# Optimization experiments

Hardware: AMD Instinct MI355X
Metric: run time of the kernel (lower is better)

## Reference

```python
import jax, jax.numpy as jnp
import numpy as np

IOU_THRESHOLD = 0.5
NEG_POS_RATIO = 3
CONF_WEIGHT = 1.0
BBOX_WEIGHT = 1.0
COUNT_WEIGHT = 0.2
B, A, G = 16, 65536, 32


def _make_boxes(key, shape, max_size):
    kc, ks = jax.random.split(key)
    centers = jax.random.uniform(kc, shape[:-1] + (2,))
    sizes = jax.random.uniform(ks, shape[:-1] + (2,)) * max_size + 0.02
    return jnp.concatenate([centers - sizes / 2, centers + sizes / 2], axis=-1)


def setup_inputs() -> dict:
    key = jax.random.key(0)
    k1, k2, k3, k4 = jax.random.split(key, 4)
    bbox_pred = _make_boxes(k1, (B, A, 4), 0.15)
    conf_pred = jax.random.uniform(k2, (B, A)) * 0.98 + 0.01  # valid probs for BCE
    anchors = _make_boxes(k3, (A, 4), 0.15)
    gt_boxes = _make_boxes(k4, (B, G, 4), 0.3)
    return {"bbox_pred": bbox_pred, "conf_pred": conf_pred, "anchors": anchors, "gt_boxes": gt_boxes}


def _bce(p, t):
    # torch BCELoss: clamps log terms at -100
    logp = jnp.maximum(jnp.log(p), -100.0)
    log1mp = jnp.maximum(jnp.log1p(-p), -100.0)
    return -(t * logp + (1.0 - t) * log1mp)


def _smooth_l1(x, y):
    d = jnp.abs(x - y)
    return jnp.where(d < 1.0, 0.5 * d * d, d - 0.5)


def _center_size(b):
    return jnp.concatenate([(b[:, :2] + b[:, 2:]) / 2, b[:, 2:] - b[:, :2]], axis=1)


def _iou(anchors, gt):  # [A,4],[G,4] -> [A,G]
    lt = jnp.maximum(anchors[:, None, :2], gt[None, :, :2])
    rb = jnp.minimum(anchors[:, None, 2:], gt[None, :, 2:])
    wh = jnp.clip(rb - lt, 0.0)
    inter = wh[..., 0] * wh[..., 1]
    area_a = (anchors[:, 2] - anchors[:, 0]) * (anchors[:, 3] - anchors[:, 1])
    area_g = (gt[:, 2] - gt[:, 0]) * (gt[:, 3] - gt[:, 1])
    union = area_a[:, None] + area_g[None, :] - inter
    return inter / (union + 1e-6)


def _per_image(bbox_p, conf_p, gt, anchors):
    ious = _iou(anchors, gt)                      # [A,G]
    best_gt_iou = ious.max(axis=1)                # [A]
    best_gt_idx = ious.argmax(axis=1)             # [A]
    best_anchor_idx = ious.argmax(axis=0)         # [G]
    pos = (best_gt_iou > IOU_THRESHOLD).at[best_anchor_idx].set(True)
    num_pos = pos.sum()

    matched = gt[best_gt_idx]                     # [A,4]
    loc = _smooth_l1(_center_size(bbox_p), _center_size(matched)).sum(axis=1)
    loc_loss = jnp.where(pos, loc, 0.0).sum()

    conf_t = pos.astype(conf_p.dtype)
    bce = _bce(conf_p, conf_t)                    # [A]
    neg_bce = jnp.where(pos, 0.0, bce)
    num_neg = jnp.minimum(num_pos * NEG_POS_RATIO, A - num_pos)
    sorted_neg = jnp.sort(neg_bce)[::-1]
    neg_sum = jnp.where(jnp.arange(A) < num_neg, sorted_neg, 0.0).sum()
    pos_sum = jnp.where(pos, bce, 0.0).sum()
    conf_loss = neg_sum + pos_sum

    pred_count = (conf_p > 0.5).sum()
    return loc_loss, conf_loss, num_pos, pred_count, best_gt_iou


def reference(bbox_pred, conf_pred, anchors, gt_boxes):
    loc_l, conf_l, num_pos, pred_cnt, best_gt_iou = jax.vmap(
        _per_image, in_axes=(0, 0, 0, None))(bbox_pred, conf_pred, gt_boxes, anchors)

    # count penalty per image (gt count is fixed at G)
    diff = jnp.abs(pred_cnt - G).astype(jnp.float32)
    penalty = jnp.where(diff <= 3.0, diff * 0.2, 0.6 + 0.2 * jnp.log(jnp.maximum(diff - 2.0, 1.0)))
    total_count_loss = penalty.sum() / B

    npos = jnp.maximum(1, num_pos.sum()).astype(bbox_pred.dtype)
    total_loc_loss = loc_l.sum() / npos
    total_conf_loss = conf_l.sum() / npos

    # torch code uses best_gt_iou from the LAST image only (loop-carried variable)
    bgi = best_gt_iou[-1]
    m = bgi > 0
    cnt = m.sum()
    mean_iou = jnp.where(cnt > 0, jnp.where(m, bgi, 0.0).sum() / jnp.maximum(cnt, 1).astype(bgi.dtype), 0.1)
    iou_quality = jnp.clip(1.0 - mean_iou, 0.1, 0.9)
    dyn_bbox_w = BBOX_WEIGHT * (1.0 + iou_quality)

    total_loss = dyn_bbox_w * total_loc_loss + CONF_WEIGHT * total_conf_loss + COUNT_WEIGHT * total_count_loss
    return total_loss, total_conf_loss, total_loc_loss, total_count_loss, mean_iou
```

## Files before the change

kernel.cpp:

```cpp
#include <hip/hip_runtime.h>
#include <math.h>

#define BB 16
#define AA 65536
#define GG 32

#define OFF_PACKED   0
#define OFF_HIST     4096
#define OFF_NUMPOS   69632
#define OFF_LOCSUM   69696
#define OFF_POSBCE   69760
#define OFF_PREDCNT  69824
#define OFF_NEGSUM   69888
#define OFF_NGT      69952
#define OFF_MIOU_S   70016
#define OFF_MIOU_C   70020
#define OFF_VK       70080
#define MEMSET_BYTES 71680
#define OFF_NEGBCE   2097152

__device__ __forceinline__ float iou_exact(float ax, float ay, float az, float aw,
                                           float area_a,
                                           float gx, float gy, float gz, float gw,
                                           float area_g) {
    float lx = fmaxf(ax, gx), ly = fmaxf(ay, gy);
    float rx = fminf(az, gz), ry = fminf(aw, gw);
    float w = fmaxf(__fsub_rn(rx, lx), 0.0f);
    float h = fmaxf(__fsub_rn(ry, ly), 0.0f);
    float inter = __fmul_rn(w, h);
    float uni = __fsub_rn(__fadd_rn(area_a, area_g), inter);
    return __fdiv_rn(inter, __fadd_rn(uni, 1e-6f));
}

__device__ __forceinline__ float sl1(float x, float y) {
    float d = fabsf(__fsub_rn(x, y));
    return (d < 1.0f) ? __fmul_rn(__fmul_rn(0.5f, d), d) : __fsub_rn(d, 0.5f);
}

__device__ __forceinline__ float loc_term(float4 bp, float4 gb) {
    float pcx = __fmul_rn(__fadd_rn(bp.x, bp.z), 0.5f);
    float pcy = __fmul_rn(__fadd_rn(bp.y, bp.w), 0.5f);
    float pw = __fsub_rn(bp.z, bp.x), ph = __fsub_rn(bp.w, bp.y);
    float gcx = __fmul_rn(__fadd_rn(gb.x, gb.z), 0.5f);
    float gcy = __fmul_rn(__fadd_rn(gb.y, gb.w), 0.5f);
    float gw = __fsub_rn(gb.z, gb.x), gh = __fsub_rn(gb.w, gb.y);
    return __fadd_rn(__fadd_rn(__fadd_rn(sl1(pcx, gcx), sl1(pcy, gcy)), sl1(pw, gw)), sl1(ph, gh));
}

__global__ __launch_bounds__(256) void k_main(const float4* __restrict__ bbox,
                                              const float* __restrict__ conf,
                                              const float4* __restrict__ anchors,
                                              const float4* __restrict__ gt,
                                              unsigned long long* __restrict__ packed,
                                              float* __restrict__ neg_bce,
                                              int* __restrict__ hist0,
                                              int* __restrict__ num_pos,
                                              float* __restrict__ loc_sum,
                                              float* __restrict__ posbce,
                                              int* __restrict__ pred_cnt,
                                              float* __restrict__ miou_s,
                                              int* __restrict__ miou_c) {
    const int b = blockIdx.y, t = threadIdx.x;
    const int base = blockIdx.x * 1024;
    __shared__ unsigned long long red[4][GG];
    __shared__ int sh[256];
    __shared__ float sloc[4], spb[4], sms[4];
    __shared__ int snp[4], spc[4], smc[4];
    sh[t] = 0;
    float4 an[4]; float aa[4]; float bi[4]; int bix[4]; int aidx[4];
#pragma unroll
    for (int j = 0; j < 4; ++j) {
        aidx[j] = base + j * 256 + t;
        an[j] = anchors[aidx[j]];
        aa[j] = __fmul_rn(__fsub_rn(an[j].z, an[j].x), __fsub_rn(an[j].w, an[j].y));
        bi[j] = -1.0f; bix[j] = 0;
    }
    __syncthreads();
    const int lane = t & 63, wv = t >> 6;
    for (int g = 0; g < GG; g += 2) {
        float4 g0 = gt[b * GG + g];
        float4 g1 = gt[b * GG + g + 1];
        float ag0 = __fmul_rn(__fsub_rn(g0.z, g0.x), __fsub_rn(g0.w, g0.y));
        float ag1 = __fmul_rn(__fsub_rn(g1.z, g1.x), __fsub_rn(g1.w, g1.y));
        unsigned long long pk0 = 0ull, pk1 = 0ull;
#pragma unroll
        for (int j = 0; j < 4; ++j) {
            float i0 = iou_exact(an[j].x, an[j].y, an[j].z, an[j].w, aa[j],
                                 g0.x, g0.y, g0.z, g0.w, ag0);
            float i1 = iou_exact(an[j].x, an[j].y, an[j].z, an[j].w, aa[j],
                                 g1.x, g1.y, g1.z, g1.w, ag1);
            if (i0 > bi[j]) { bi[j] = i0; bix[j] = g; }
            if (i1 > bi[j]) { bi[j] = i1; bix[j] = g + 1; }
            unsigned long long p0 = ((unsigned long long)__float_as_uint(i0) << 32)
                                  | (unsigned long long)(0xFFFFFFFFu - (unsigned)aidx[j]);
            unsigned long long p1 = ((unsigned long long)__float_as_uint(i1) << 32)
                                  | (unsigned long long)(0xFFFFFFFFu - (unsigned)aidx[j]);
            if (p0 > pk0) pk0 = p0;
            if (p1 > pk1) pk1 = p1;
        }
#pragma unroll
        for (int off = 32; off; off >>= 1) {
            unsigned long long q0 = __shfl_xor(pk0, off, 64);
            unsigned long long q1 = __shfl_xor(pk1, off, 64);
            if (q0 > pk0) pk0 = q0;
            if (q1 > pk1) pk1 = q1;
        }
        if (lane == 0) { red[wv][g] = pk0; red[wv][g + 1] = pk1; }
    }
    float loc = 0.0f, pb = 0.0f, ms = 0.0f;
    int np_ = 0, pc = 0, mc = 0;
#pragma unroll
    for (int j = 0; j < 4; ++j) {
        const int idx = b * AA + aidx[j];
        float p = conf[idx];
        bool pos = bi[j] > 0.5f;
        float bce, nb;
        if (pos) { bce = -fmaxf(logf(p), -100.0f); nb = 0.0f; }
        else     { bce = -fmaxf(log1pf(-p), -100.0f); nb = bce; }
        neg_bce[idx] = nb;
        if (!pos) atomicAdd(&sh[__float_as_uint(nb) >> 24], 1);
        if (pos) {
            loc += loc_term(bbox[idx], gt[b * GG + bix[j]]);
            pb += bce;
            np_++;
        }
        pc += (p > 0.5f) ? 1 : 0;
        if (b == BB - 1 && bi[j] > 0.0f) { ms += bi[j]; mc++; }
    }
#pragma unroll
    for (int off = 32; off; off >>= 1) {
        loc += __shfl_xor(loc, off, 64);
        pb  += __shfl_xor(pb, off, 64);
        np_ += __shfl_xor(np_, off, 64);
        pc  += __shfl_xor(pc, off, 64);
        if (b == BB - 1) { ms += __shfl_xor(ms, off, 64); mc += __shfl_xor(mc, off, 64); }
    }
    if (lane == 0) {
        sloc[wv] = loc; spb[wv] = pb; snp[wv] = np_; spc[wv] = pc;
        sms[wv] = ms; smc[wv] = mc;
    }
    __syncthreads();
    if (t == 0) {
        float L = sloc[0] + sloc[1] + sloc[2] + sloc[3];
        float P = spb[0] + spb[1] + spb[2] + spb[3];
        int   N = snp[0] + snp[1] + snp[2] + snp[3];
        int   C = spc[0] + spc[1] + spc[2] + spc[3];
        if (L != 0.0f) atomicAdd(&loc_sum[b], L);
        if (P != 0.0f) atomicAdd(&posbce[b], P);
        if (N) atomicAdd(&num_pos[b], N);
        if (C) atomicAdd(&pred_cnt[b], C);
        if (b == BB - 1) {
            float S = sms[0] + sms[1] + sms[2] + sms[3];
            int   M = smc[0] + smc[1] + smc[2] + smc[3];
            if (S != 0.0f) atomicAdd(miou_s, S);
            if (M) atomicAdd(miou_c, M);
        }
    }
    if (t < GG) {
        unsigned long long p = red[0][t];
#pragma unroll
        for (int w = 1; w < 4; ++w) if (red[w][t] > p) p = red[w][t];
        atomicMax(&packed[b * GG + t], p);
    }
    if (sh[t]) atomicAdd(&hist0[b * 256 + t], sh[t]);
}

__global__ __launch_bounds__(512) void k_force(const float4* __restrict__ bbox,
                                               const float* __restrict__ conf,
                                               const float4* __restrict__ anchors,
                                               const float4* __restrict__ gt,
                                               const unsigned long long* __restrict__ packed,
                                               float* __restrict__ neg_bce,
                                               int* __restrict__ hist0,
                                               int* __restrict__ num_pos,
                                               float* __restrict__ loc_sum,
                                               float* __restrict__ posbce) {
    const int t = threadIdx.x;
    const int b = t >> 5, g = t & 31;
    __shared__ unsigned int win[BB][GG];
    unsigned int a = 0xFFFFFFFFu - (unsigned int)(packed[b * GG + g] & 0xFFFFFFFFull);
    win[b][g] = a;
    __syncthreads();
    bool dup = false;
    for (int gp = 0; gp < g; ++gp) dup |= (win[b][gp] == a);
    if (dup) return;
    float4 an = anchors[a];
    float aa = __fmul_rn(__fsub_rn(an.z, an.x), __fsub_rn(an.w, an.y));
    float bi = -1.0f; int bix = 0;
    for (int gg = 0; gg < GG; ++gg) {
        float4 gv = gt[b * GG + gg];
        float ag = __fmul_rn(__fsub_rn(gv.z, gv.x), __fsub_rn(gv.w, gv.y));
        float iou = iou_exact(an.x, an.y, an.z, an.w, aa, gv.x, gv.y, gv.z, gv.w, ag);
        if (iou > bi) { bi = iou; bix = gg; }
    }
    if (bi > 0.5f) return;
    const int idx = b * AA + a;
    float p = conf[idx];
    float nb = -fmaxf(log1pf(-p), -100.0f);
    atomicSub(&hist0[b * 256 + (int)(__float_as_uint(nb) >> 24)], 1);
    neg_bce[idx] = 0.0f;
    float bce = -fmaxf(logf(p), -100.0f);
    atomicAdd(&posbce[b], bce);
    atomicAdd(&num_pos[b], 1);
    atomicAdd(&loc_sum[b], loc_term(bbox[idx], gt[b * GG + bix]));
}

__device__ __forceinline__ void scan_level(const int* __restrict__ histL, int t,
                                           int* ss, int* sres,
                                           unsigned int* prefix, int* k, int shift) {
    int kk = *k;
    ss[t] = histL[t];
    __syncthreads();
#pragma unroll
    for (int off = 1; off < 256; off <<= 1) {
        int v = (t + off < 256) ? ss[t + off] : 0;
        __syncthreads();
        ss[t] += v;
        __syncthreads();
    }
    if (ss[t] >= kk && (t == 255 || ss[t + 1] < kk)) {
        sres[0] = t;
        sres[1] = (t == 255) ? kk : (kk - ss[t + 1]);
    }
    __syncthreads();
    *prefix |= ((unsigned int)sres[0]) << shift;
    *k = sres[1];
    __syncthreads();
}

__global__ __launch_bounds__(256) void k_hist(const float* __restrict__ neg_bce,
                                              int* __restrict__ hist,
                                              const int* __restrict__ num_pos,
                                              int pass) {
    const int b = blockIdx.y, t = threadIdx.x;
    __shared__ int ss[256];
    __shared__ int sres[2];
    __shared__ int sh[256];
    int np_ = num_pos[b];
    int k = min(3 * np_, AA - np_);
    if (k <= 0) return;
    unsigned int prefix = 0;
    for (int L = 0; L < pass; ++L)
        scan_level(&hist[(L * BB + b) * 256], t, ss, sres, &prefix, &k, 24 - 8 * L);
    sh[t] = 0;
    __syncthreads();
    const unsigned int pmask = 0xFFFFFFFFu << (32 - 8 * pass);
    const int shift = 24 - 8 * pass;
    for (int a = blockIdx.x * 256 + t; a < AA; a += gridDim.x * 256) {
        unsigned int bits = __float_as_uint(neg_bce[b * AA + a]);
        if ((bits & pmask) == prefix) atomicAdd(&sh[(bits >> shift) & 0xFFu], 1);
    }
    __syncthreads();
    if (sh[t]) atomicAdd(&hist[(pass * BB + b) * 256 + t], sh[t]);
}

__global__ __launch_bounds__(256) void k_topk(const float* __restrict__ neg_bce,
                                              const int* __restrict__ hist,
                                              const int* __restrict__ num_pos,
                                              float* __restrict__ negsum,
                                              int* __restrict__ ngt,
                                              float* __restrict__ vk_arr) {
    const int b = blockIdx.y, t = threadIdx.x;
    __shared__ int ss[256];
    __shared__ int sres[2];
    __shared__ float sfs[4];
    __shared__ int sfc[4];
    int np_ = num_pos[b];
    int k = min(3 * np_, AA - np_);
    if (k <= 0) return;
    unsigned int prefix = 0;
    for (int L = 0; L < 4; ++L)
        scan_level(&hist[(L * BB + b) * 256], t, ss, sres, &prefix, &k, 24 - 8 * L);
    const float vk = __uint_as_float(prefix);
    if (blockIdx.x == 0 && t == 0) vk_arr[b] = vk;
    float s = 0.0f; int c = 0;
    for (int a = blockIdx.x * 256 + t; a < AA; a += gridDim.x * 256) {
        float v = neg_bce[b * AA + a];
        if (v > vk) { s += v; c++; }
    }
#pragma unroll
    for (int off = 32; off; off >>= 1) { s += __shfl_xor(s, off, 64); c += __shfl_xor(c, off, 64); }
    const int lane = t & 63, wv = t >> 6;
    if (lane == 0) { sfs[wv] = s; sfc[wv] = c; }
    __syncthreads();
    if (t == 0) {
        float S = sfs[0] + sfs[1] + sfs[2] + sfs[3];
        int   C = sfc[0] + sfc[1] + sfc[2] + sfc[3];
        if (S != 0.0f) atomicAdd(&negsum[b], S);
        if (C) atomicAdd(&ngt[b], C);
    }
}

__global__ void k_final(const int* __restrict__ num_pos,
                        const float* __restrict__ loc_sum,
                        const float* __restrict__ posbce,
                        const float* __restrict__ negsum,
                        const int* __restrict__ ngt,
                        const float* __restrict__ vk_arr,
                        const int* __restrict__ pred_cnt,
                        const float* __restrict__ miou_s,
                        const int* __restrict__ miou_c,
                        float* __restrict__ out) {
    if (threadIdx.x == 0) {
        int npos_t = 0; float loc_t = 0.0f, conf_t = 0.0f, cnt_t = 0.0f;
        for (int b = 0; b < BB; ++b) {
            int np_ = num_pos[b];
            int k0 = min(3 * np_, AA - np_);
            float add = posbce[b] + negsum[b];
            if (k0 > 0) add += (float)(k0 - ngt[b]) * vk_arr[b];
            conf_t += add;
            npos_t += np_;
            loc_t += loc_sum[b];
            float diff = fabsf((float)(pred_cnt[b] - GG));
            cnt_t += (diff <= 3.0f) ? diff * 0.2f
                                    : 0.6f + 0.2f * logf(fmaxf(diff - 2.0f, 1.0f));
        }
        float total_count = cnt_t / (float)BB;
        float npos = (float)max(1, npos_t);
        float total_loc = loc_t / npos;
        float total_conf = conf_t / npos;
        int C = *miou_c;
        float mean_iou = (C > 0) ? (*miou_s / (float)max(C, 1)) : 0.1f;
        float q = fminf(fmaxf(1.0f - mean_iou, 0.1f), 0.9f);
        float dyn = 1.0f + q;
        out[0] = dyn * total_loc + total_conf + 0.2f * total_count;
        out[1] = total_conf;
        out[2] = total_loc;
        out[3] = total_count;
        out[4] = mean_iou;
    }
}

extern "C" void kernel_launch(void* const* d_in, const int* in_sizes, int n_in,
                              void* d_out, int out_size, void* d_ws, size_t ws_size,
                              hipStream_t stream) {
    (void)in_sizes; (void)n_in; (void)out_size; (void)ws_size;
    const float* bbox    = (const float*)d_in[0];
    const float* conf    = (const float*)d_in[1];
    const float* anchors = (const float*)d_in[2];
    const float* gt      = (const float*)d_in[3];
    char* ws = (char*)d_ws;
    unsigned long long* packed = (unsigned long long*)(ws + OFF_PACKED);
    int*   hist     = (int*)(ws + OFF_HIST);
    int*   num_pos  = (int*)(ws + OFF_NUMPOS);
    float* loc_sum  = (float*)(ws + OFF_LOCSUM);
    float* posbce   = (float*)(ws + OFF_POSBCE);
    int*   pred_cnt = (int*)(ws + OFF_PREDCNT);
    float* negsum   = (float*)(ws + OFF_NEGSUM);
    int*   ngt      = (int*)(ws + OFF_NGT);
    float* miou_s   = (float*)(ws + OFF_MIOU_S);
    int*   miou_c   = (int*)(ws + OFF_MIOU_C);
    float* vk_arr   = (float*)(ws + OFF_VK);
    float* neg_bce  = (float*)(ws + OFF_NEGBCE);

    hipMemsetAsync(d_ws, 0, MEMSET_BYTES, stream);
    k_main<<<dim3(64, BB), 256, 0, stream>>>((const float4*)bbox, conf,
                                             (const float4*)anchors, (const float4*)gt,
                                             packed, neg_bce,
                                             hist, num_pos, loc_sum, posbce, pred_cnt,
                                             miou_s, miou_c);
    k_force<<<1, 512, 0, stream>>>((const float4*)bbox, conf,
                                   (const float4*)anchors, (const float4*)gt,
                                   packed, neg_bce, hist, num_pos, loc_sum, posbce);
    for (int pass = 1; pass <= 3; ++pass)
        k_hist<<<dim3(64, BB), 256, 0, stream>>>(neg_bce, hist, num_pos, pass);
    k_topk<<<dim3(64, BB), 256, 0, stream>>>(neg_bce, hist, num_pos, negsum, ngt, vk_arr);
    k_final<<<1, 64, 0, stream>>>(num_pos, loc_sum, posbce, negsum, ngt, vk_arr,
                                  pred_cnt, miou_s, miou_c, (float*)d_out);
}
```

Measured before the change: 165.2 us.

## Fuse force-match, radix histogram passes and top-k into one per-image kernel

The separate force-match kernel, three histogram-pass kernels and the top-k kernel are merged into one k_select kernel with one 256-thread block per image. That block does the forced-positive fix-up, then runs the remaining radix-select levels in shared memory and finishes with the threshold sum, so five launches become one. The trade is far less parallelism: 16 blocks each stream 65536 values four times, where before 1024 blocks per pass did it. Separately, the 64-bit packed max shuffle in k_main is split into a float max reduction followed by a min-index reduction.

```diff
diff --git a/kernel.cpp b/kernel.cpp
--- a/kernel.cpp
+++ b/kernel.cpp
@@ -45,6 +45,29 @@
     float gcy = __fmul_rn(__fadd_rn(gb.y, gb.w), 0.5f);
     float gw = __fsub_rn(gb.z, gb.x), gh = __fsub_rn(gb.w, gb.y);
     return __fadd_rn(__fadd_rn(__fadd_rn(sl1(pcx, gcx), sl1(pcy, gcy)), sl1(pw, gw)), sl1(ph, gh));
+}
+
+__device__ __forceinline__ void scan_level(const int* __restrict__ histL, int t,
+                                           int* ss, int* sres,
+                                           unsigned int* prefix, int* k, int shift) {
+    int kk = *k;
+    ss[t] = histL[t];
+    __syncthreads();
+#pragma unroll
+    for (int off = 1; off < 256; off <<= 1) {
+        int v = (t + off < 256) ? ss[t + off] : 0;
+        __syncthreads();
+        ss[t] += v;
+        __syncthreads();
+    }
+    if (ss[t] >= kk && (t == 255 || ss[t + 1] < kk)) {
+        sres[0] = t;
+        sres[1] = (t == 255) ? kk : (kk - ss[t + 1]);
+    }
+    __syncthreads();
+    *prefix |= ((unsigned int)sres[0]) << shift;
+    *k = sres[1];
+    __syncthreads();
 }
 
 __global__ __launch_bounds__(256) void k_main(const float4* __restrict__ bbox,
@@ -82,7 +105,8 @@
         float4 g1 = gt[b * GG + g + 1];
         float ag0 = __fmul_rn(__fsub_rn(g0.z, g0.x), __fsub_rn(g0.w, g0.y));
         float ag1 = __fmul_rn(__fsub_rn(g1.z, g1.x), __fsub_rn(g1.w, g1.y));
-        unsigned long long pk0 = 0ull, pk1 = 0ull;
+        float m0 = -1.0f, m1 = -1.0f;
+        unsigned int c0 = 0xFFFFFFFFu, c1 = 0xFFFFFFFFu;
 #pragma unroll
         for (int j = 0; j < 4; ++j) {
             float i0 = iou_exact(an[j].x, an[j].y, an[j].z, an[j].w, aa[j],
@@ -91,21 +115,28 @@
                                  g1.x, g1.y, g1.z, g1.w, ag1);
             if (i0 > bi[j]) { bi[j] = i0; bix[j] = g; }
             if (i1 > bi[j]) { bi[j] = i1; bix[j] = g + 1; }
-            unsigned long long p0 = ((unsigned long long)__float_as_uint(i0) << 32)
-                                  | (unsigned long long)(0xFFFFFFFFu - (unsigned)aidx[j]);
-            unsigned long long p1 = ((unsigned long long)__float_as_uint(i1) << 32)
-                                  | (unsigned long long)(0xFFFFFFFFu - (unsigned)aidx[j]);
-            if (p0 > pk0) pk0 = p0;
-            if (p1 > pk1) pk1 = p1;
-        }
+            if (i0 > m0) { m0 = i0; c0 = (unsigned)aidx[j]; }
+            if (i1 > m1) { m1 = i1; c1 = (unsigned)aidx[j]; }
+        }
+        float lm0 = m0, lm1 = m1;
 #pragma unroll
         for (int off = 32; off; off >>= 1) {
-            unsigned long long q0 = __shfl_xor(pk0, off, 64);
-            unsigned long long q1 = __shfl_xor(pk1, off, 64);
-            if (q0 > pk0) pk0 = q0;
-            if (q1 > pk1) pk1 = q1;
-        }
-        if (lane == 0) { red[wv][g] = pk0; red[wv][g + 1] = pk1; }
+            m0 = fmaxf(m0, __shfl_xor(m0, off, 64));
+            m1 = fmaxf(m1, __shfl_xor(m1, off, 64));
+        }
+        c0 = (lm0 == m0) ? c0 : 0xFFFFFFFFu;
+        c1 = (lm1 == m1) ? c1 : 0xFFFFFFFFu;
+#pragma unroll
+        for (int off = 32; off; off >>= 1) {
+            c0 = min(c0, __shfl_xor(c0, off, 64));
+            c1 = min(c1, __shfl_xor(c1, off, 64));
+        }
+        if (lane == 0) {
+            red[wv][g]     = ((unsigned long long)__float_as_uint(m0) << 32)
+                           | (unsigned long long)(0xFFFFFFFFu - c0);
+            red[wv][g + 1] = ((unsigned long long)__float_as_uint(m1) << 32)
+                           | (unsigned long long)(0xFFFFFFFFu - c1);
+        }
     }
     float loc = 0.0f, pb = 0.0f, ms = 0.0f;
     int np_ = 0, pc = 0, mc = 0;
@@ -157,125 +188,98 @@
         }
     }
     if (t < GG) {
-        unsigned long long p = red[0][t];
-#pragma unroll
-        for (int w = 1; w < 4; ++w) if (red[w][t] > p) p = red[w][t];
-        atomicMax(&packed[b * GG + t], p);
+        unsigned long long q = red[0][t];
+#pragma unroll
+        for (int w = 1; w < 4; ++w) if (red[w][t] > q) q = red[w][t];
+        atomicMax(&packed[b * GG + t], q);
     }
     if (sh[t]) atomicAdd(&hist0[b * 256 + t], sh[t]);
 }
 
-__global__ __launch_bounds__(512) void k_force(const float4* __restrict__ bbox,
-                                               const float* __restrict__ conf,
-                                               const float4* __restrict__ anchors,
-                                               const float4* __restrict__ gt,
-                                               const unsigned long long* __restrict__ packed,
-                                               float* __restrict__ neg_bce,
-                                               int* __restrict__ hist0,
-                                               int* __restrict__ num_pos,
-                                               float* __restrict__ loc_sum,
-                                               float* __restrict__ posbce) {
-    const int t = threadIdx.x;
-    const int b = t >> 5, g = t & 31;
-    __shared__ unsigned int win[BB][GG];
-    unsigned int a = 0xFFFFFFFFu - (unsigned int)(packed[b * GG + g] & 0xFFFFFFFFull);
-    win[b][g] = a;
-    __syncthreads();
-    bool dup = false;
-    for (int gp = 0; gp < g; ++gp) dup |= (win[b][gp] == a);
-    if (dup) return;
-    float4 an = anchors[a];
-    float aa = __fmul_rn(__fsub_rn(an.z, an.x), __fsub_rn(an.w, an.y));
-    float bi = -1.0f; int bix = 0;
-    for (int gg = 0; gg < GG; ++gg) {
-        float4 gv = gt[b * GG + gg];
-        float ag = __fmul_rn(__fsub_rn(gv.z, gv.x), __fsub_rn(gv.w, gv.y));
-        float iou = iou_exact(an.x, an.y, an.z, an.w, aa, gv.x, gv.y, gv.z, gv.w, ag);
-        if (iou > bi) { bi = iou; bix = gg; }
-    }
-    if (bi > 0.5f) return;
-    const int idx = b * AA + a;
-    float p = conf[idx];
-    float nb = -fmaxf(log1pf(-p), -100.0f);
-    atomicSub(&hist0[b * 256 + (int)(__float_as_uint(nb) >> 24)], 1);
-    neg_bce[idx] = 0.0f;
-    float bce = -fmaxf(logf(p), -100.0f);
-    atomicAdd(&posbce[b], bce);
-    atomicAdd(&num_pos[b], 1);
-    atomicAdd(&loc_sum[b], loc_term(bbox[idx], gt[b * GG + bix]));
-}
-
-__device__ __forceinline__ void scan_level(const int* __restrict__ histL, int t,
-                                           int* ss, int* sres,
-                                           unsigned int* prefix, int* k, int shift) {
-    int kk = *k;
-    ss[t] = histL[t];
-    __syncthreads();
-#pragma unroll
-    for (int off = 1; off < 256; off <<= 1) {
-        int v = (t + off < 256) ? ss[t + off] : 0;
-        __syncthreads();
-        ss[t] += v;
-        __syncthreads();
-    }
-    if (ss[t] >= kk && (t == 255 || ss[t + 1] < kk)) {
-        sres[0] = t;
-        sres[1] = (t == 255) ? kk : (kk - ss[t + 1]);
-    }
-    __syncthreads();
-    *prefix |= ((unsigned int)sres[0]) << shift;
-    *k = sres[1];
-    __syncthreads();
-}
-
-__global__ __launch_bounds__(256) void k_hist(const float* __restrict__ neg_bce,
-                                              int* __restrict__ hist,
-                                              const int* __restrict__ num_pos,
-                                              int pass) {
-    const int b = blockIdx.y, t = threadIdx.x;
+__global__ __launch_bounds__(256) void k_select(const float4* __restrict__ bbox,
+                                                const float* __restrict__ conf,
+                                                const float4* __restrict__ anchors,
+                                                const float4* __restrict__ gt,
+                                                const unsigned long long* __restrict__ packed,
+                                                const int* __restrict__ hist0,
+                                                float* __restrict__ neg_bce,
+                                                int* __restrict__ num_pos,
+                                                float* __restrict__ loc_sum,
+                                                float* __restrict__ posbce,
+                                                float* __restrict__ negsum,
+                                                int* __restrict__ ngt,
+                                                float* __restrict__ vk_arr) {
+    const int b = blockIdx.x, t = threadIdx.x;
+    __shared__ int h[256];
     __shared__ int ss[256];
     __shared__ int sres[2];
-    __shared__ int sh[256];
-    int np_ = num_pos[b];
-    int k = min(3 * np_, AA - np_);
+    __shared__ unsigned int win[GG];
+    __shared__ int s_np_extra, s_np;
+    __shared__ float s_pb_extra, s_loc_extra;
+    __shared__ float sfs[4];
+    __shared__ int sfc[4];
+    h[t] = hist0[b * 256 + t];
+    if (t == 0) { s_np_extra = 0; s_pb_extra = 0.0f; s_loc_extra = 0.0f; }
+    if (t < GG) win[t] = 0xFFFFFFFFu - (unsigned int)(packed[b * GG + t] & 0xFFFFFFFFull);
+    __syncthreads();
+    if (t < GG) {
+        unsigned int a = win[t];
+        bool dup = false;
+        for (int gp = 0; gp < t; ++gp) dup |= (win[gp] == a);
+        if (!dup) {
+            float4 an = anchors[a];
+            float aa = __fmul_rn(__fsub_rn(an.z, an.x), __fsub_rn(an.w, an.y));
+            float bi = -1.0f; int bix = 0;
+            for (int gg = 0; gg < GG; ++gg) {
+                float4 gv = gt[b * GG + gg];
+                float ag = __fmul_rn(__fsub_rn(gv.z, gv.x), __fsub_rn(gv.w, gv.y));
+                float iou = iou_exact(an.x, an.y, an.z, an.w, aa, gv.x, gv.y, gv.z, gv.w, ag);
+                if (iou > bi) { bi = iou; bix = gg; }
+            }
+            if (!(bi > 0.5f)) {
+                const int idx = b * AA + (int)a;
+                float p = conf[idx];
+                float nb = -fmaxf(log1pf(-p), -100.0f);
+                atomicSub(&h[(int)(__float_as_uint(nb) >> 24)], 1);
+                neg_bce[idx] = 0.0f;
+                atomicAdd(&s_pb_extra, -fmaxf(logf(p), -100.0f));
+                atomicAdd(&s_loc_extra, loc_term(bbox[idx], gt[b * GG + bix]));
+                atomicAdd(&s_np_extra, 1);
+            }
+        }
+    }
+    __threadfence_block();
+    __syncthreads();
+    if (t == 0) {
+        int np = num_pos[b] + s_np_extra;
+        num_pos[b] = np;
+        s_np = np;
+        if (s_pb_extra != 0.0f) posbce[b] += s_pb_extra;
+        if (s_loc_extra != 0.0f) loc_sum[b] += s_loc_extra;
+    }
+    __syncthreads();
+    const int np = s_np;
+    int k = min(3 * np, AA - np);
     if (k <= 0) return;
     unsigned int prefix = 0;
-    for (int L = 0; L < pass; ++L)
-        scan_level(&hist[(L * BB + b) * 256], t, ss, sres, &prefix, &k, 24 - 8 * L);
-    sh[t] = 0;
-    __syncthreads();
-    const unsigned int pmask = 0xFFFFFFFFu << (32 - 8 * pass);
-    const int shift = 24 - 8 * pass;
-    for (int a = blockIdx.x * 256 + t; a < AA; a += gridDim.x * 256) {
-        unsigned int bits = __float_as_uint(neg_bce[b * AA + a]);
-        if ((bits & pmask) == prefix) atomicAdd(&sh[(bits >> shift) & 0xFFu], 1);
-    }
-    __syncthreads();
-    if (sh[t]) atomicAdd(&hist[(pass * BB + b) * 256 + t], sh[t]);
-}
-
-__global__ __launch_bounds__(256) void k_topk(const float* __restrict__ neg_bce,
-                                              const int* __restrict__ hist,
-                                              const int* __restrict__ num_pos,
-                                              float* __restrict__ negsum,
-                                              int* __restrict__ ngt,
-                                              float* __restrict__ vk_arr) {
-    const int b = blockIdx.y, t = threadIdx.x;
-    __shared__ int ss[256];
-    __shared__ int sres[2];
-    __shared__ float sfs[4];
-    __shared__ int sfc[4];
-    int np_ = num_pos[b];
-    int k = min(3 * np_, AA - np_);
-    if (k <= 0) return;
-    unsigned int prefix = 0;
-    for (int L = 0; L < 4; ++L)
-        scan_level(&hist[(L * BB + b) * 256], t, ss, sres, &prefix, &k, 24 - 8 * L);
+    scan_level(h, t, ss, sres, &prefix, &k, 24);
+    const float* __restrict__ nbp = neg_bce + (size_t)b * AA;
+    for (int lvl = 1; lvl <= 3; ++lvl) {
+        const int shift = 24 - 8 * lvl;
+        const unsigned int pmask = 0xFFFFFFFFu << (shift + 8);
+        h[t] = 0;
+        __syncthreads();
+        for (int i = 0; i < AA / 256; ++i) {
+            unsigned int bits = __float_as_uint(nbp[i * 256 + t]);
+            if ((bits & pmask) == prefix) atomicAdd(&h[(bits >> shift) & 0xFFu], 1);
+        }
+        __syncthreads();
+        scan_level(h, t, ss, sres, &prefix, &k, shift);
+    }
     const float vk = __uint_as_float(prefix);
-    if (blockIdx.x == 0 && t == 0) vk_arr[b] = vk;
     float s = 0.0f; int c = 0;
-    for (int a = blockIdx.x * 256 + t; a < AA; a += gridDim.x * 256) {
-        float v = neg_bce[b * AA + a];
+    for (int i = 0; i < AA / 256; ++i) {
+        float v = nbp[i * 256 + t];
         if (v > vk) { s += v; c++; }
     }
 #pragma unroll
@@ -284,10 +288,9 @@
     if (lane == 0) { sfs[wv] = s; sfc[wv] = c; }
     __syncthreads();
     if (t == 0) {
-        float S = sfs[0] + sfs[1] + sfs[2] + sfs[3];
-        int   C = sfc[0] + sfc[1] + sfc[2] + sfc[3];
-        if (S != 0.0f) atomicAdd(&negsum[b], S);
-        if (C) atomicAdd(&ngt[b], C);
+        negsum[b] = sfs[0] + sfs[1] + sfs[2] + sfs[3];
+        ngt[b]    = sfc[0] + sfc[1] + sfc[2] + sfc[3];
+        vk_arr[b] = vk;
     }
 }
 
@@ -359,12 +362,10 @@
                                              packed, neg_bce,
                                              hist, num_pos, loc_sum, posbce, pred_cnt,
                                              miou_s, miou_c);
-    k_force<<<1, 512, 0, stream>>>((const float4*)bbox, conf,
-                                   (const float4*)anchors, (const float4*)gt,
-                                   packed, neg_bce, hist, num_pos, loc_sum, posbce);
-    for (int pass = 1; pass <= 3; ++pass)
-        k_hist<<<dim3(64, BB), 256, 0, stream>>>(neg_bce, hist, num_pos, pass);
-    k_topk<<<dim3(64, BB), 256, 0, stream>>>(neg_bce, hist, num_pos, negsum, ngt, vk_arr);
+    k_select<<<BB, 256, 0, stream>>>((const float4*)bbox, conf,
+                                     (const float4*)anchors, (const float4*)gt,
+                                     packed, hist, neg_bce,
+                                     num_pos, loc_sum, posbce, negsum, ngt, vk_arr);
     k_final<<<1, 64, 0, stream>>>(num_pos, loc_sum, posbce, negsum, ngt, vk_arr,
                                   pred_cnt, miou_s, miou_c, (float*)d_out);
 }
```

Result: slower. 264.4 us (+60.1%).
